# Performance work log

Measured on AMD Instinct MI355X. Metric: run time of the kernel, lower is better.

The kernel has to match this reference:

```python
import jax, jax.numpy as jnp
import numpy as np

K = 9  # 3x3 kernel taps

def conv2d(x, w, b):
    # stride 1, padding 1, NCHW / OIHW
    out = jax.lax.conv_general_dilated(x, w, (1, 1), ((1, 1), (1, 1)),
                                       dimension_numbers=('NCHW', 'OIHW', 'NCHW'))
    return out + b[None, :, None, None]

def deform_conv2d(x, offset, mask, w, b):
    # torchvision modulated deformable conv, kernel 3x3, stride 1, pad 1, dilation 1
    B, C, H, W = x.shape
    off = offset.reshape(B, K, 2, H, W)  # per-tap (dy, dx)
    ii = (jnp.arange(K) // 3).astype(x.dtype) - 1.0  # kernel row offset (pad=1)
    jj = (jnp.arange(K) % 3).astype(x.dtype) - 1.0   # kernel col offset
    hh = jnp.arange(H, dtype=x.dtype)[None, None, :, None]
    ww = jnp.arange(W, dtype=x.dtype)[None, None, None, :]
    py = hh + ii[None, :, None, None] + off[:, :, 0]  # [B,K,H,W] sample rows
    px = ww + jj[None, :, None, None] + off[:, :, 1]  # [B,K,H,W] sample cols

    y0 = jnp.floor(py); x0 = jnp.floor(px)
    dy = py - y0; dx = px - x0
    y0 = y0.astype(jnp.int32); x0 = x0.astype(jnp.int32)

    xf = x.reshape(B, C, H * W)

    def gather(yi, xi):
        valid = ((yi >= 0) & (yi < H) & (xi >= 0) & (xi < W)).astype(x.dtype)
        yc = jnp.clip(yi, 0, H - 1)
        xc = jnp.clip(xi, 0, W - 1)
        idx = (yc * W + xc).reshape(B, K * H * W)
        v = jax.vmap(lambda xb, ib: xb[:, ib])(xf, idx)  # [B,C,K*H*W]
        return v.reshape(B, C, K, H, W) * valid[:, None]

    v00 = gather(y0,     x0)
    v01 = gather(y0,     x0 + 1)
    v10 = gather(y0 + 1, x0)
    v11 = gather(y0 + 1, x0 + 1)

    dy = dy[:, None]; dx = dx[:, None]  # broadcast over channel dim
    val = (v00 * (1 - dy) * (1 - dx) + v01 * (1 - dy) * dx
           + v10 * dy * (1 - dx) + v11 * dy * dx)
    val = val * mask[:, None]  # sigmoid modulation, [B,1,K,H,W]

    out = jnp.einsum('ock,bckhw->bohw', w.reshape(w.shape[0], C, K), val)
    return out + b[None, :, None, None]

def setup_inputs() -> dict:
    key = jax.random.key(0)
    k1, k2, k3 = jax.random.split(key, 3)
    x = jax.random.normal(k1, (8, 3, 512, 512), dtype=jnp.float32)
    w_off = jax.random.normal(k2, (27, 3, 3, 3), dtype=jnp.float32) * 0.05
    b_off = jnp.zeros((27,), dtype=jnp.float32)
    w_def = jax.random.normal(k3, (3, 3, 3, 3), dtype=jnp.float32) * 0.1
    b_def = jnp.zeros((3,), dtype=jnp.float32)
    return {'x': x, 'w_off': w_off, 'b_off': b_off, 'w_def': w_def, 'b_def': b_def}

def reference(x, w_off, b_off, w_def, b_def):
    ow = conv2d(x, w_off, b_off)            # [B,27,H,W]
    offset = ow[:, :18]                      # 2*9 offsets
    mask = jax.nn.sigmoid(ow[:, 18:])        # 9 modulation masks
    return deform_conv2d(x, offset, mask, w_def, b_def)
```

## Files before the change

### kernel.cpp

```cpp
#include <hip/hip_runtime.h>
#include <math.h>

#define BN 8
#define CIN 3
#define HH 512
#define WW 512
#define KK 9
#define OC 3
#define OFFC 27
#define PATCH 27

__global__ __launch_bounds__(256) void deform_fused_kernel(
    const float* __restrict__ x,
    const float* __restrict__ w_off,
    const float* __restrict__ b_off,
    const float* __restrict__ w_def,
    const float* __restrict__ b_def,
    float* __restrict__ out)
{
    __shared__ float s_woff[OFFC * PATCH];
    __shared__ float s_boff[OFFC];
    __shared__ float s_wdef[OC * PATCH];
    __shared__ float s_bdef[OC];

    for (int i = threadIdx.x; i < OFFC * PATCH; i += blockDim.x) s_woff[i] = w_off[i];
    if (threadIdx.x < OFFC)       s_boff[threadIdx.x] = b_off[threadIdx.x];
    if (threadIdx.x < OC * PATCH) s_wdef[threadIdx.x] = w_def[threadIdx.x];
    if (threadIdx.x < OC)         s_bdef[threadIdx.x] = b_def[threadIdx.x];
    __syncthreads();

    const int w = blockIdx.x * blockDim.x + threadIdx.x;
    const int h = blockIdx.y;
    const int b = blockIdx.z;
    if (w >= WW) return;

    const float* xb = x + (size_t)b * CIN * HH * WW;

    float patch[PATCH];
    #pragma unroll
    for (int c = 0; c < CIN; ++c) {
        const float* xp = xb + (size_t)c * HH * WW;
        #pragma unroll
        for (int t = 0; t < KK; ++t) {
            const int yy = h + t / 3 - 1;
            const int xx = w + t % 3 - 1;
            const bool in = (yy >= 0) & (yy < HH) & (xx >= 0) & (xx < WW);
            patch[c * KK + t] = in ? xp[yy * WW + xx] : 0.0f;
        }
    }

    float acc0 = s_bdef[0];
    float acc1 = s_bdef[1];
    float acc2 = s_bdef[2];

    #pragma unroll 1
    for (int k = 0; k < KK; ++k) {
        float oy = s_boff[2 * k];
        float ox = s_boff[2 * k + 1];
        float om = s_boff[18 + k];
        const float* wy = &s_woff[(2 * k) * PATCH];
        const float* wx = &s_woff[(2 * k + 1) * PATCH];
        const float* wm = &s_woff[(18 + k) * PATCH];
        #pragma unroll
        for (int i = 0; i < PATCH; ++i) {
            const float p = patch[i];
            oy = fmaf(wy[i], p, oy);
            ox = fmaf(wx[i], p, ox);
            om = fmaf(wm[i], p, om);
        }

        const float m = 1.0f / (1.0f + __expf(-om));

        const float py = (float)h + (float)(k / 3 - 1) + oy;
        const float px = (float)w + (float)(k % 3 - 1) + ox;
        const float y0f = floorf(py);
        const float x0f = floorf(px);
        const float dy = py - y0f;
        const float dx = px - x0f;
        const int y0 = (int)y0f;
        const int x0 = (int)x0f;

        const float w00 = (1.0f - dy) * (1.0f - dx);
        const float w01 = (1.0f - dy) * dx;
        const float w10 = dy * (1.0f - dx);
        const float w11 = dy * dx;

        const bool vy0 = (y0 >= 0)     & (y0 < HH);
        const bool vy1 = (y0 + 1 >= 0) & (y0 + 1 < HH);
        const bool vx0 = (x0 >= 0)     & (x0 < WW);
        const bool vx1 = (x0 + 1 >= 0) & (x0 + 1 < WW);

        const int yc0 = min(max(y0, 0), HH - 1);
        const int yc1 = min(max(y0 + 1, 0), HH - 1);
        const int xc0 = min(max(x0, 0), WW - 1);
        const int xc1 = min(max(x0 + 1, 0), WW - 1);

        #pragma unroll
        for (int c = 0; c < CIN; ++c) {
            const float* xp = xb + (size_t)c * HH * WW;
            const float v00 = (vy0 & vx0) ? xp[yc0 * WW + xc0] : 0.0f;
            const float v01 = (vy0 & vx1) ? xp[yc0 * WW + xc1] : 0.0f;
            const float v10 = (vy1 & vx0) ? xp[yc1 * WW + xc0] : 0.0f;
            const float v11 = (vy1 & vx1) ? xp[yc1 * WW + xc1] : 0.0f;

            float val = v00 * w00 + v01 * w01 + v10 * w10 + v11 * w11;
            val *= m;

            acc0 = fmaf(s_wdef[0 * PATCH + c * KK + k], val, acc0);
            acc1 = fmaf(s_wdef[1 * PATCH + c * KK + k], val, acc1);
            acc2 = fmaf(s_wdef[2 * PATCH + c * KK + k], val, acc2);
        }
    }

    const size_t plane = (size_t)HH * WW;
    const size_t base = (size_t)b * OC * plane + (size_t)h * WW + w;
    out[base]             = acc0;
    out[base + plane]     = acc1;
    out[base + 2 * plane] = acc2;
}

extern "C" void kernel_launch(void* const* d_in, const int* in_sizes, int n_in,
                              void* d_out, int out_size, void* d_ws, size_t ws_size,
                              hipStream_t stream) {
    const float* x     = (const float*)d_in[0];
    const float* w_off = (const float*)d_in[1];
    const float* b_off = (const float*)d_in[2];
    const float* w_def = (const float*)d_in[3];
    const float* b_def = (const float*)d_in[4];
    float* out = (float*)d_out;

    dim3 block(256, 1, 1);
    dim3 grid(WW / 256, HH, BN);
    deform_fused_kernel<<<grid, block, 0, stream>>>(x, w_off, b_off, w_def, b_def, out);
}
```

Before: 222.3 us.

## Hoist offset conv out of tap loop with packed FMA and fast interior gather path

A small pre-kernel reorders the offset-conv weights into interleaved pairs in workspace. The main kernel now computes all 27 offset/mask channels in one fully unrolled pass using packed two-wide FMAs, with weights read as uniform scalar loads instead of from LDS. The tap loop is fully unrolled and adds a wave-uniform fast path that, when every sampled 2x2 neighbourhood is in bounds, uses two-wide unaligned vector loads and skips clamping and masking. Costs are an extra kernel launch, more register pressure from 26 live accumulators, and the fallback path is still needed for border waves.

```diff
diff --git a/kernel.cpp b/kernel.cpp
--- a/kernel.cpp
+++ b/kernel.cpp
@@ -1,38 +1,42 @@
 #include <hip/hip_runtime.h>
 #include <math.h>
+
+typedef float f2 __attribute__((ext_vector_type(2)));
+typedef float f2u __attribute__((ext_vector_type(2), aligned(4)));
 
 #define BN 8
 #define CIN 3
 #define HH 512
 #define WW 512
 #define KK 9
-#define OC 3
 #define OFFC 27
 #define PATCH 27
+#define NPAIR 13
+
+__global__ void reorder_weights(const float* __restrict__ w_off, float* __restrict__ ws)
+{
+    const int t = threadIdx.x;
+    if (t < PATCH * NPAIR) {
+        const int i = t / NPAIR, q = t % NPAIR;
+        ws[2 * t]     = w_off[(2 * q) * PATCH + i];
+        ws[2 * t + 1] = w_off[(2 * q + 1) * PATCH + i];
+    }
+    if (t < PATCH) {
+        ws[2 * PATCH * NPAIR + t] = w_off[26 * PATCH + t];
+    }
+}
 
 __global__ __launch_bounds__(256) void deform_fused_kernel(
     const float* __restrict__ x,
-    const float* __restrict__ w_off,
+    const float* __restrict__ wsw,
     const float* __restrict__ b_off,
     const float* __restrict__ w_def,
     const float* __restrict__ b_def,
     float* __restrict__ out)
 {
-    __shared__ float s_woff[OFFC * PATCH];
-    __shared__ float s_boff[OFFC];
-    __shared__ float s_wdef[OC * PATCH];
-    __shared__ float s_bdef[OC];
-
-    for (int i = threadIdx.x; i < OFFC * PATCH; i += blockDim.x) s_woff[i] = w_off[i];
-    if (threadIdx.x < OFFC)       s_boff[threadIdx.x] = b_off[threadIdx.x];
-    if (threadIdx.x < OC * PATCH) s_wdef[threadIdx.x] = w_def[threadIdx.x];
-    if (threadIdx.x < OC)         s_bdef[threadIdx.x] = b_def[threadIdx.x];
-    __syncthreads();
-
     const int w = blockIdx.x * blockDim.x + threadIdx.x;
     const int h = blockIdx.y;
     const int b = blockIdx.z;
-    if (w >= WW) return;
 
     const float* xb = x + (size_t)b * CIN * HH * WW;
 
@@ -49,25 +53,37 @@
         }
     }
 
-    float acc0 = s_bdef[0];
-    float acc1 = s_bdef[1];
-    float acc2 = s_bdef[2];
+    f2 owp[NPAIR];
+    #pragma unroll
+    for (int q = 0; q < NPAIR; ++q) {
+        owp[q].x = b_off[2 * q];
+        owp[q].y = b_off[2 * q + 1];
+    }
+    float ow26 = b_off[26];
 
-    #pragma unroll 1
+    #pragma unroll
+    for (int i = 0; i < PATCH; ++i) {
+        const float p = patch[i];
+        const f2 pp = { p, p };
+        const f2* wrow = (const f2*)(wsw + i * (2 * NPAIR));
+        #pragma unroll
+        for (int q = 0; q < NPAIR; ++q) {
+            owp[q] = __builtin_elementwise_fma(wrow[q], pp, owp[q]);
+        }
+        ow26 = fmaf(wsw[2 * PATCH * NPAIR + i], p, ow26);
+    }
+
+    float acc0 = b_def[0];
+    float acc1 = b_def[1];
+    float acc2 = b_def[2];
+
+    #pragma unroll
     for (int k = 0; k < KK; ++k) {
-        float oy = s_boff[2 * k];
-        float ox = s_boff[2 * k + 1];
-        float om = s_boff[18 + k];
-        const float* wy = &s_woff[(2 * k) * PATCH];
-        const float* wx = &s_woff[(2 * k + 1) * PATCH];
-        const float* wm = &s_woff[(18 + k) * PATCH];
-        #pragma unroll
-        for (int i = 0; i < PATCH; ++i) {
-            const float p = patch[i];
-            oy = fmaf(wy[i], p, oy);
-            ox = fmaf(wx[i], p, ox);
-            om = fmaf(wm[i], p, om);
-        }
+        const float oy = owp[k].x;
+        const float ox = owp[k].y;
+        const float om = (k < 8) ? ((k & 1) ? owp[9 + (k >> 1)].y
+                                            : owp[9 + (k >> 1)].x)
+                                 : ow26;
 
         const float m = 1.0f / (1.0f + __expf(-om));
 
@@ -80,40 +96,55 @@
         const int y0 = (int)y0f;
         const int x0 = (int)x0f;
 
-        const float w00 = (1.0f - dy) * (1.0f - dx);
-        const float w01 = (1.0f - dy) * dx;
-        const float w10 = dy * (1.0f - dx);
-        const float w11 = dy * dx;
+        const f2 wTop = { (1.0f - dy) * (1.0f - dx), (1.0f - dy) * dx };
+        const f2 wBot = { dy * (1.0f - dx), dy * dx };
 
-        const bool vy0 = (y0 >= 0)     & (y0 < HH);
-        const bool vy1 = (y0 + 1 >= 0) & (y0 + 1 < HH);
-        const bool vx0 = (x0 >= 0)     & (x0 < WW);
-        const bool vx1 = (x0 + 1 >= 0) & (x0 + 1 < WW);
+        const int fast = (y0 >= 0) & (y0 + 1 < HH) & (x0 >= 0) & (x0 + 1 < WW);
 
-        const int yc0 = min(max(y0, 0), HH - 1);
-        const int yc1 = min(max(y0 + 1, 0), HH - 1);
-        const int xc0 = min(max(x0, 0), WW - 1);
-        const int xc1 = min(max(x0 + 1, 0), WW - 1);
+        if (__all(fast)) {
+            const int idx = y0 * WW + x0;
+            #pragma unroll
+            for (int c = 0; c < CIN; ++c) {
+                const float* xp = xb + (size_t)c * HH * WW + idx;
+                const f2 vT = *(const f2u*)(xp);
+                const f2 vB = *(const f2u*)(xp + WW);
+                const f2 s = vT * wTop + vB * wBot;
+                const float val = (s.x + s.y) * m;
+                acc0 = fmaf(w_def[0 * PATCH + c * KK + k], val, acc0);
+                acc1 = fmaf(w_def[1 * PATCH + c * KK + k], val, acc1);
+                acc2 = fmaf(w_def[2 * PATCH + c * KK + k], val, acc2);
+            }
+        } else {
+            const bool vy0 = (y0 >= 0)     & (y0 < HH);
+            const bool vy1 = (y0 + 1 >= 0) & (y0 + 1 < HH);
+            const bool vx0 = (x0 >= 0)     & (x0 < WW);
+            const bool vx1 = (x0 + 1 >= 0) & (x0 + 1 < WW);
 
-        #pragma unroll
-        for (int c = 0; c < CIN; ++c) {
-            const float* xp = xb + (size_t)c * HH * WW;
-            const float v00 = (vy0 & vx0) ? xp[yc0 * WW + xc0] : 0.0f;
-            const float v01 = (vy0 & vx1) ? xp[yc0 * WW + xc1] : 0.0f;
-            const float v10 = (vy1 & vx0) ? xp[yc1 * WW + xc0] : 0.0f;
-            const float v11 = (vy1 & vx1) ? xp[yc1 * WW + xc1] : 0.0f;
+            const int yc0 = min(max(y0, 0), HH - 1);
+            const int yc1 = min(max(y0 + 1, 0), HH - 1);
+            const int xc0 = min(max(x0, 0), WW - 1);
+            const int xc1 = min(max(x0 + 1, 0), WW - 1);
 
-            float val = v00 * w00 + v01 * w01 + v10 * w10 + v11 * w11;
-            val *= m;
+            #pragma unroll
+            for (int c = 0; c < CIN; ++c) {
+                const float* xp = xb + (size_t)c * HH * WW;
+                const float v00 = (vy0 & vx0) ? xp[yc0 * WW + xc0] : 0.0f;
+                const float v01 = (vy0 & vx1) ? xp[yc0 * WW + xc1] : 0.0f;
+                const float v10 = (vy1 & vx0) ? xp[yc1 * WW + xc0] : 0.0f;
+                const float v11 = (vy1 & vx1) ? xp[yc1 * WW + xc1] : 0.0f;
 
-            acc0 = fmaf(s_wdef[0 * PATCH + c * KK + k], val, acc0);
-            acc1 = fmaf(s_wdef[1 * PATCH + c * KK + k], val, acc1);
-            acc2 = fmaf(s_wdef[2 * PATCH + c * KK + k], val, acc2);
+                const float val =
+                    (v00 * wTop.x + v01 * wTop.y + v10 * wBot.x + v11 * wBot.y) * m;
+
+                acc0 = fmaf(w_def[0 * PATCH + c * KK + k], val, acc0);
+                acc1 = fmaf(w_def[1 * PATCH + c * KK + k], val, acc1);
+                acc2 = fmaf(w_def[2 * PATCH + c * KK + k], val, acc2);
+            }
         }
     }
 
     const size_t plane = (size_t)HH * WW;
-    const size_t base = (size_t)b * OC * plane + (size_t)h * WW + w;
+    const size_t base = (size_t)b * (CIN * plane) + (size_t)h * WW + w;
     out[base]             = acc0;
     out[base + plane]     = acc1;
     out[base + 2 * plane] = acc2;
@@ -128,8 +159,11 @@
     const float* w_def = (const float*)d_in[3];
     const float* b_def = (const float*)d_in[4];
     float* out = (float*)d_out;
+    float* wsw = (float*)d_ws;
+
+    reorder_weights<<<1, 512, 0, stream>>>(w_off, wsw);
 
     dim3 block(256, 1, 1);
     dim3 grid(WW / 256, HH, BN);
-    deform_fused_kernel<<<grid, block, 0, stream>>>(x, w_off, b_off, w_def, b_def, out);
+    deform_fused_kernel<<<grid, block, 0, stream>>>(x, wsw, b_off, w_def, b_def, out);
 }
```

Result: slower. 436.6 us (+96.4%).
